# Kernel optimization log

Measured on AMD Instinct MI355X. Metric: run time of the kernel, lower is better.

Reference implementation:

```python
import jax, jax.numpy as jnp
import numpy as np

D_MODEL = 1024
NUM_HEADS = 16
D_HEAD = D_MODEL // NUM_HEADS
B, T = 2, 2048


def setup_inputs() -> dict:
    key = jax.random.key(0)
    kx, kq, kk, kv, ko = jax.random.split(key, 5)
    # xavier_uniform bound for square (D,D) linear weights
    bound = float(np.sqrt(6.0 / (D_MODEL + D_MODEL)))
    uni = lambda k: jax.random.uniform(k, (D_MODEL, D_MODEL), jnp.float32, -bound, bound)
    return {
        "x": jax.random.normal(kx, (B, T, D_MODEL), jnp.float32),
        "Wq": uni(kq),
        "Wk": uni(kk),
        "Wv": uni(kv),
        "Wo": uni(ko),
    }


def _split_heads(x):
    # (B, T, D) -> (B, H, T, d_head)
    b, t, _ = x.shape
    return x.reshape(b, t, NUM_HEADS, D_HEAD).transpose(0, 2, 1, 3)


def _exclusive_output_mod(Y, V):
    dt = V.dtype
    tiny = jnp.asarray(jnp.finfo(dt).tiny, dt)
    eps = jnp.asarray(jnp.finfo(dt).eps, dt)
    v_sq = jnp.sum(V * V, axis=-1, keepdims=True)
    y_dot_v = jnp.sum(Y * V, axis=-1, keepdims=True)
    scale = jnp.where(v_sq > 0, y_dot_v / jnp.maximum(v_sq, tiny), jnp.zeros_like(y_dot_v))
    Z = Y - scale * V
    residual_norm = jnp.linalg.norm(Z, axis=-1, keepdims=True)
    reference_norm = jnp.maximum(
        jnp.linalg.norm(Y, axis=-1, keepdims=True),
        jnp.linalg.norm(V, axis=-1, keepdims=True),
    )
    cleanup_tol = eps * Z.shape[-1] * reference_norm
    return jnp.where((v_sq > 0) & (residual_norm <= cleanup_tol), jnp.zeros_like(Z), Z)


def reference(x, Wq, Wk, Wv, Wo):
    Q = _split_heads(x @ Wq.T)  # (B,H,T,dh)
    K = _split_heads(x @ Wk.T)
    V = _split_heads(x @ Wv.T)
    sm_scale = 1.0 / np.sqrt(D_HEAD)
    scores = jnp.einsum("bhqd,bhkd->bhqk", Q, K) * sm_scale
    P = jax.nn.softmax(scores, axis=-1)
    Y = jnp.einsum("bhqk,bhkd->bhqd", P, V)
    Z = _exclusive_output_mod(Y, V)
    # merge heads: (B,H,T,dh) -> (B,T,D)
    Zm = Z.transpose(0, 2, 1, 3).reshape(x.shape[0], x.shape[1], D_MODEL)
    return Zm @ Wo.T
```

## Files before the change

### kernel.cpp

```cpp
#include <hip/hip_runtime.h>
#include <math.h>

#define DM   1024
#define TTOK 2048
#define NTOK 4096

typedef __bf16 bf16x8 __attribute__((ext_vector_type(8)));
typedef __bf16 bf16x4 __attribute__((ext_vector_type(4)));
typedef __bf16 bf16x2 __attribute__((ext_vector_type(2)));
typedef float  f32x4  __attribute__((ext_vector_type(4)));
typedef float  f32x16 __attribute__((ext_vector_type(16)));

#define QSCALE 0.18033688011112042f

#if defined(__has_builtin)
#if __has_builtin(__builtin_amdgcn_exp2f)
#define EXP2F(x) __builtin_amdgcn_exp2f(x)
#endif
#endif
#ifndef EXP2F
#define EXP2F(x) exp2f(x)
#endif

#define GLDS16(g, l) __builtin_amdgcn_global_load_lds( \
    (__attribute__((address_space(1))) void*)(g),      \
    (__attribute__((address_space(3))) void*)(l), 16, 0, 0)

__device__ __forceinline__ unsigned pk2(float a, float b) {
    bf16x2 t; t[0] = (__bf16)a; t[1] = (__bf16)b;
    return __builtin_bit_cast(unsigned, t);
}
union FU { unsigned u[4]; bf16x8 v; };

__global__ __launch_bounds__(256)
void cvt_all(const float* __restrict__ x,  const float* __restrict__ Wq,
             const float* __restrict__ Wk, const float* __restrict__ Wv,
             const float* __restrict__ Wo, __bf16* __restrict__ dst) {
    size_t g = ((size_t)blockIdx.x * 256 + threadIdx.x) * 8;
    const float* s;
    size_t off;
    const size_t NX = (size_t)NTOK * DM;
    if (g < NX) { s = x; off = g; }
    else {
        size_t gg = g - NX;
        int w = (int)(gg >> 20);
        off = gg & ((1u << 20) - 1);
        s = (w == 0) ? Wq : (w == 1) ? Wk : (w == 2) ? Wv : Wo;
    }
    float4 a = *(const float4*)(s + off);
    float4 b = *(const float4*)(s + off + 4);
    bf16x8 v;
    v[0] = (__bf16)a.x; v[1] = (__bf16)a.y; v[2] = (__bf16)a.z; v[3] = (__bf16)a.w;
    v[4] = (__bf16)b.x; v[5] = (__bf16)b.y; v[6] = (__bf16)b.z; v[7] = (__bf16)b.w;
    *(bf16x8*)(dst + g) = v;
}

#define LSTR 136
#define DBUF 8192

__global__ __launch_bounds__(256)
void gemm_qkv(const __bf16* __restrict__ X,
              const __bf16* __restrict__ W0, const __bf16* __restrict__ W1,
              const __bf16* __restrict__ W2,
              __bf16* __restrict__ Oq, __bf16* __restrict__ Ok,
              __bf16* __restrict__ Ovt)
{
    const int z = blockIdx.z;
    const __bf16 *A, *B;
    int m0, n0;
    if (z < 2) {
        A = z ? W1 : W0; B = X;
        m0 = blockIdx.y * 128; n0 = blockIdx.x * 128;
    } else {
        A = X; B = W2;
        m0 = blockIdx.x * 128; n0 = blockIdx.y * 128;
    }

    __shared__ __attribute__((aligned(16))) __bf16 smem[128 * LSTR];

    const int tid  = threadIdx.x;
    const int lane = tid & 63;
    const int wave = tid >> 6;
    const int wm = wave & 1, wn = wave >> 1;
    const int col = lane & 15, quad = lane >> 4;

    const __bf16* Ag = A + (size_t)(m0 + (tid >> 2)) * DM + (tid & 3) * 8;
    const __bf16* Bg = B + (size_t)(n0 + (tid >> 2)) * DM + (tid & 3) * 8;
    __bf16* lA = smem + tid * 8;
    __bf16* lB = smem + 4096 + tid * 8;

    f32x4 acc[4][4];
#pragma unroll
    for (int i = 0; i < 4; ++i)
#pragma unroll
        for (int j = 0; j < 4; ++j)
#pragma unroll
            for (int r = 0; r < 4; ++r) acc[i][j][r] = 0.0f;

    GLDS16(Ag,                   lA);
    GLDS16(Ag + (size_t)64 * DM, lA + 2048);
    GLDS16(Bg,                   lB);
    GLDS16(Bg + (size_t)64 * DM, lB + 2048);
    __syncthreads();

    const int nk = DM / 32;
    for (int t = 0; t < nk; ++t) {
        const int cur = (t & 1) * DBUF;
        const int nxt = DBUF - cur;

        if (t + 1 < nk) {
            const int k1 = (t + 1) * 32;
            GLDS16(Ag + k1,                   lA + nxt);
            GLDS16(Ag + (size_t)64 * DM + k1, lA + nxt + 2048);
            GLDS16(Bg + k1,                   lB + nxt);
            GLDS16(Bg + (size_t)64 * DM + k1, lB + nxt + 2048);
        }

        const __bf16* Asr = smem + cur;
        const __bf16* Bsr = smem + cur + 4096;
        bf16x8 af[4], bfr[4];
#pragma unroll
        for (int i = 0; i < 4; ++i)
            af[i] = *(const bf16x8*)&Asr[(wm * 64 + i * 16 + col) * 32 + quad * 8];
#pragma unroll
        for (int j = 0; j < 4; ++j)
            bfr[j] = *(const bf16x8*)&Bsr[(wn * 64 + j * 16 + col) * 32 + quad * 8];
#pragma unroll
        for (int i = 0; i < 4; ++i)
#pragma unroll
            for (int j = 0; j < 4; ++j)
                acc[i][j] = __builtin_amdgcn_mfma_f32_16x16x32_bf16(af[i], bfr[j], acc[i][j], 0, 0, 0);

        __syncthreads();
    }

    const float sc = (z == 0) ? QSCALE : 1.0f;
#pragma unroll
    for (int i = 0; i < 4; ++i)
#pragma unroll
        for (int j = 0; j < 4; ++j) {
            const int ml = wm * 64 + i * 16 + quad * 4;
            const int nl = wn * 64 + j * 16 + col;
            bf16x4 pk;
#pragma unroll
            for (int r = 0; r < 4; ++r) pk[r] = (__bf16)(acc[i][j][r] * sc);
            *(bf16x4*)&smem[nl * LSTR + ml] = pk;
        }
    __syncthreads();

#pragma unroll
    for (int it = 0; it < 8; ++it) {
        int c   = tid + 256 * it;
        int row = c >> 4;
        int ch  = (c & 15) * 8;
        bf16x8 v = *(const bf16x8*)&smem[row * LSTR + ch];
        if (z < 2) {
            int t  = n0 + row;
            int b  = t >> 11; t &= 2047;
            int hd = m0 + ch;
            int h  = hd >> 6, d = hd & 63;
            *(bf16x8*)&((z ? Ok : Oq)[(((size_t)(b * 16 + h)) * TTOK + t) * 64 + d]) = v;
        } else {
            int hd = n0 + row;
            int h  = hd >> 6, d = hd & 63;
            int t  = m0 + ch;
            int b  = t >> 11; t &= 2047;
            *(bf16x8*)&Ovt[(((size_t)(b * 16 + h)) * 64 + d) * TTOK + t] = v;
        }
    }
}

#define ODBUF 6144

__global__ __launch_bounds__(256)
void gemm_oproj(const __bf16* __restrict__ X, const __bf16* __restrict__ Wo,
                float* __restrict__ Of)
{
    const int f = blockIdx.x + 8 * blockIdx.y;
    const int c = f & 7, i0 = f >> 3;
    const int m0 = (8 * c + (i0 & 7)) * 64;
    const int n0 = (i0 >> 3) * 128;

    __shared__ __attribute__((aligned(16))) __bf16 smem[2 * ODBUF];

    const int tid  = threadIdx.x;
    const int lane = tid & 63;
    const int wave = tid >> 6;
    const int col = lane & 15, quad = lane >> 4;

    const __bf16* Ag = X  + (size_t)(m0 + (tid >> 2)) * DM + (tid & 3) * 8;
    const __bf16* Bg = Wo + (size_t)(n0 + (tid >> 2)) * DM + (tid & 3) * 8;
    __bf16* lA = smem + tid * 8;
    __bf16* lB = smem + 2048 + tid * 8;

    f32x4 acc[4][2];
#pragma unroll
    for (int i = 0; i < 4; ++i)
#pragma unroll
        for (int j = 0; j < 2; ++j)
#pragma unroll
            for (int r = 0; r < 4; ++r) acc[i][j][r] = 0.0f;

    GLDS16(Ag,                   lA);
    GLDS16(Bg,                   lB);
    GLDS16(Bg + (size_t)64 * DM, lB + 2048);
    __syncthreads();

    const int nk = DM / 32;
    for (int t = 0; t < nk; ++t) {
        const int cur = (t & 1) * ODBUF;
        const int nxt = ODBUF - cur;
        if (t + 1 < nk) {
            const int k1 = (t + 1) * 32;
            GLDS16(Ag + k1,                   lA + nxt);
            GLDS16(Bg + k1,                   lB + nxt);
            GLDS16(Bg + (size_t)64 * DM + k1, lB + nxt + 2048);
        }
        const __bf16* Asr = smem + cur;
        const __bf16* Bsr = smem + cur + 2048;
        bf16x8 af[4], bfr[2];
#pragma unroll
        for (int i = 0; i < 4; ++i)
            af[i] = *(const bf16x8*)&Asr[(i * 16 + col) * 32 + quad * 8];
#pragma unroll
        for (int j = 0; j < 2; ++j)
            bfr[j] = *(const bf16x8*)&Bsr[(wave * 32 + j * 16 + col) * 32 + quad * 8];
#pragma unroll
        for (int i = 0; i < 4; ++i)
#pragma unroll
            for (int j = 0; j < 2; ++j)
                acc[i][j] = __builtin_amdgcn_mfma_f32_16x16x32_bf16(af[i], bfr[j], acc[i][j], 0, 0, 0);
        __syncthreads();
    }

#pragma unroll
    for (int i = 0; i < 4; ++i)
#pragma unroll
        for (int j = 0; j < 2; ++j) {
            const int mb = m0 + i * 16 + quad * 4;
            const int n  = n0 + wave * 32 + j * 16 + col;
#pragma unroll
            for (int r = 0; r < 4; ++r)
                Of[(size_t)(mb + r) * DM + n] = acc[i][j][r];
        }
}

__global__ __launch_bounds__(256)
void attn_mfma(const __bf16* __restrict__ Qg, const __bf16* __restrict__ Kg,
               const __bf16* __restrict__ Vtg, __bf16* __restrict__ Zm)
{
    const int bh = blockIdx.y;
    const int q0 = blockIdx.x * 128;
    const size_t base = (size_t)bh * TTOK * 64;

    __shared__ __attribute__((aligned(16))) __bf16 Ks[2][64 * 72];
    __shared__ __attribute__((aligned(16))) __bf16 Vs[2][64 * 72];

    const int tid  = threadIdx.x;
    const int lane = tid & 63, wave = tid >> 6;
    const int c32  = lane & 31, h32 = lane >> 5;

    bf16x8 qf[4];
    const __bf16* qrow = Qg + base + (size_t)(q0 + wave * 32 + c32) * 64 + h32 * 8;
#pragma unroll
    for (int st = 0; st < 4; ++st)
        qf[st] = *(const bf16x8*)(qrow + st * 16);

    f32x16 O[2];
#pragma unroll
    for (int r = 0; r < 16; ++r) { O[0][r] = 0.0f; O[1][r] = 0.0f; }
    float lsum = 0.0f;

    const int rs = tid >> 2, soff = (tid & 3) * 16;

    bf16x8 kr0 = *(const bf16x8*)(Kg  + base + (size_t)rs * 64 + soff);
    bf16x8 kr1 = *(const bf16x8*)(Kg  + base + (size_t)rs * 64 + soff + 8);
    bf16x8 vr0 = *(const bf16x8*)(Vtg + base + (size_t)rs * TTOK + soff);
    bf16x8 vr1 = *(const bf16x8*)(Vtg + base + (size_t)rs * TTOK + soff + 8);
    *(bf16x8*)&Ks[0][rs * 72 + soff]     = kr0;
    *(bf16x8*)&Ks[0][rs * 72 + soff + 8] = kr1;
    *(bf16x8*)&Vs[0][rs * 72 + soff]     = vr0;
    *(bf16x8*)&Vs[0][rs * 72 + soff + 8] = vr1;
    {
        const __bf16* kp = Kg  + base + (size_t)(64 + rs) * 64 + soff;
        const __bf16* vp = Vtg + base + (size_t)rs * TTOK + 64 + soff;
        kr0 = *(const bf16x8*)(kp); kr1 = *(const bf16x8*)(kp + 8);
        vr0 = *(const bf16x8*)(vp); vr1 = *(const bf16x8*)(vp + 8);
    }
    __syncthreads();

    const int kb_tgt = (q0 >> 6) + (wave >> 1);
    const int qo     = (wave & 1) * 32 + c32;
    float vq[2][16];

    for (int kb = 0; kb < TTOK / 64; ++kb) {
        const int cur = kb & 1;
        const __bf16* Kc = Ks[cur];
        const __bf16* Vc = Vs[cur];

        f32x16 s0, s1;
#pragma unroll
        for (int r = 0; r < 16; ++r) { s0[r] = 0.0f; s1[r] = 0.0f; }
#pragma unroll
        for (int st = 0; st < 4; ++st) {
            bf16x8 a0 = *(const bf16x8*)&Kc[(c32)      * 72 + h32 * 8 + st * 16];
            bf16x8 a1 = *(const bf16x8*)&Kc[(32 + c32) * 72 + h32 * 8 + st * 16];
            s0 = __builtin_amdgcn_mfma_f32_32x32x16_bf16(a0, qf[st], s0, 0, 0, 0);
            s1 = __builtin_amdgcn_mfma_f32_32x32x16_bf16(a1, qf[st], s1, 0, 0, 0);
        }

        float pl0[16], pl1[16];
#pragma unroll
        for (int r = 0; r < 16; ++r) { pl0[r] = EXP2F(s0[r]); pl1[r] = EXP2F(s1[r]); }
#pragma unroll
        for (int r = 0; r < 16; ++r) lsum += pl0[r] + pl1[r];

        bf16x8 pf[4];
#pragma unroll
        for (int ks = 0; ks < 4; ++ks) {
            const float* pl = (ks & 2) ? pl1 : pl0;
            const int rb = (ks & 1) * 8;
            unsigned A0 = pk2(pl[rb + 0], pl[rb + 1]);
            unsigned A1 = pk2(pl[rb + 2], pl[rb + 3]);
            unsigned B0 = pk2(pl[rb + 4], pl[rb + 5]);
            unsigned B1 = pk2(pl[rb + 6], pl[rb + 7]);
            unsigned s0w = h32 ? A0 : B0;
            unsigned s1w = h32 ? A1 : B1;
            unsigned r0 = __shfl_xor(s0w, 32, 64);
            unsigned r1 = __shfl_xor(s1w, 32, 64);
            FU fu;
            fu.u[0] = h32 ? r0 : A0;
            fu.u[1] = h32 ? r1 : A1;
            fu.u[2] = h32 ? B0 : r0;
            fu.u[3] = h32 ? B1 : r1;
            pf[ks] = fu.v;
        }

#pragma unroll
        for (int ks = 0; ks < 4; ++ks) {
            bf16x8 v0 = *(const bf16x8*)&Vc[(c32)      * 72 + h32 * 8 + ks * 16];
            bf16x8 v1 = *(const bf16x8*)&Vc[(32 + c32) * 72 + h32 * 8 + ks * 16];
            O[0] = __builtin_amdgcn_mfma_f32_32x32x16_bf16(v0, pf[ks], O[0], 0, 0, 0);
            O[1] = __builtin_amdgcn_mfma_f32_32x32x16_bf16(v1, pf[ks], O[1], 0, 0, 0);
        }

        if (kb == kb_tgt) {
#pragma unroll
            for (int db = 0; db < 2; ++db)
#pragma unroll
                for (int rg = 0; rg < 16; ++rg) {
                    int d = db * 32 + (rg & 3) + 8 * (rg >> 2) + 4 * h32;
                    vq[db][rg] = (float)Vc[d * 72 + qo];
                }
        }

        __bf16* Kn = Ks[cur ^ 1];
        __bf16* Vn = Vs[cur ^ 1];
        *(bf16x8*)&Kn[rs * 72 + soff]     = kr0;
        *(bf16x8*)&Kn[rs * 72 + soff + 8] = kr1;
        *(bf16x8*)&Vn[rs * 72 + soff]     = vr0;
        *(bf16x8*)&Vn[rs * 72 + soff + 8] = vr1;

        {
            int kbn = (kb + 2) & (TTOK / 64 - 1);
            const __bf16* kp = Kg  + base + (size_t)(kbn * 64 + rs) * 64 + soff;
            const __bf16* vp = Vtg + base + (size_t)rs * TTOK + kbn * 64 + soff;
            kr0 = *(const bf16x8*)(kp); kr1 = *(const bf16x8*)(kp + 8);
            vr0 = *(const bf16x8*)(vp); vr1 = *(const bf16x8*)(vp + 8);
        }

        __syncthreads();
    }

    const float ltot = lsum + __shfl_xor(lsum, 32, 64);
    const float inv  = 1.0f / ltot;

    const int b = bh >> 4, h = bh & 15;
    const int q = q0 + wave * 32 + c32;
    float y[2][16];
    float yv = 0.f, v2 = 0.f, yy = 0.f;
#pragma unroll
    for (int db = 0; db < 2; ++db)
#pragma unroll
        for (int rg = 0; rg < 16; ++rg) {
            float yval = O[db][rg] * inv;
            float vval = vq[db][rg];
            y[db][rg] = yval;
            yv += yval * vval; v2 += vval * vval; yy += yval * yval;
        }
    yv += __shfl_xor(yv, 32, 64);
    v2 += __shfl_xor(v2, 32, 64);
    yy += __shfl_xor(yy, 32, 64);
    float scl = (v2 > 0.0f) ? yv / fmaxf(v2, 1.1754943508222875e-38f) : 0.0f;
    float zz = 0.f;
    float zvv[2][16];
#pragma unroll
    for (int db = 0; db < 2; ++db)
#pragma unroll
        for (int rg = 0; rg < 16; ++rg) {
            zvv[db][rg] = y[db][rg] - scl * vq[db][rg];
            zz += zvv[db][rg] * zvv[db][rg];
        }
    zz += __shfl_xor(zz, 32, 64);
    float znorm = sqrtf(zz);
    float refn  = fmaxf(sqrtf(yy), sqrtf(v2));
    bool  wipe  = (v2 > 0.0f) && (znorm <= 1.1920928955078125e-07f * 64.0f * refn);
#pragma unroll
    for (int db = 0; db < 2; ++db)
#pragma unroll
        for (int g = 0; g < 4; ++g) {
            bf16x4 pk;
#pragma unroll
            for (int r = 0; r < 4; ++r)
                pk[r] = (__bf16)(wipe ? 0.0f : zvv[db][4 * g + r]);
            int d = db * 32 + 8 * g + 4 * h32;
            *(bf16x4*)&Zm[((size_t)(b * TTOK + q)) * DM + h * 64 + d] = pk;
        }
}

extern "C" void kernel_launch(void* const* d_in, const int* in_sizes, int n_in,
                              void* d_out, int out_size, void* d_ws, size_t ws_size,
                              hipStream_t stream) {
    const float* x  = (const float*)d_in[0];
    const float* Wq = (const float*)d_in[1];
    const float* Wk = (const float*)d_in[2];
    const float* Wv = (const float*)d_in[3];
    const float* Wo = (const float*)d_in[4];

    const size_t NX = (size_t)NTOK * DM;
    const size_t NW = (size_t)DM * DM;
    __bf16* xb  = (__bf16*)d_ws;
    __bf16* wqb = xb  + NX;
    __bf16* wkb = wqb + NW;
    __bf16* wvb = wkb + NW;
    __bf16* wob = wvb + NW;
    __bf16* Qb  = wob + NW;
    __bf16* Kb  = Qb  + NX;
    __bf16* Vtb = Kb  + NX;
    __bf16* Zmb = Vtb + NX;

    cvt_all<<<(NX + 4 * NW) / 2048, 256, 0, stream>>>(x, Wq, Wk, Wv, Wo, xb);

    gemm_qkv<<<dim3(32, 8, 3), 256, 0, stream>>>(
        xb, wqb, wkb, wvb, Qb, Kb, Vtb);

    attn_mfma<<<dim3(TTOK / 128, 32), 256, 0, stream>>>(Qb, Kb, Vtb, Zmb);

    gemm_oproj<<<dim3(8, 64), 256, 0, stream>>>(Zmb, wob, (float*)d_out);
}
```

Baseline: 185.7 us.

## Split attention KV range across two wave groups and merge partial outputs via LDS

Each attention block now runs 512 threads: two groups of four waves each cover half of the key/value sequence for the same 128 queries, each with its own double-buffered LDS tiles. After the loop the second group writes its partial O accumulators and row sums to LDS and the first group adds them before normalising. The V self-row values used by the exclusive-output step are now read directly from global memory instead of being captured during the loop. The softmax exp/pack is also interleaved with the PV MFMAs. This aims to double the waves in flight per block to hide latency, at the cost of more LDS per block, an extra reduction pass, and tighter register pressure under launch_bounds(512,4).

New measurement: 184.6 us. No clear change (-0.6%).

```diff
diff --git a/kernel.cpp b/kernel.cpp
--- a/kernel.cpp
+++ b/kernel.cpp
@@ -245,7 +245,7 @@
         }
 }
 
-__global__ __launch_bounds__(256)
+__global__ __launch_bounds__(512, 4)
 void attn_mfma(const __bf16* __restrict__ Qg, const __bf16* __restrict__ Kg,
                const __bf16* __restrict__ Vtg, __bf16* __restrict__ Zm)
 {
@@ -253,15 +253,17 @@
     const int q0 = blockIdx.x * 128;
     const size_t base = (size_t)bh * TTOK * 64;
 
-    __shared__ __attribute__((aligned(16))) __bf16 Ks[2][64 * 72];
-    __shared__ __attribute__((aligned(16))) __bf16 Vs[2][64 * 72];
+    __shared__ __attribute__((aligned(16))) __bf16 lds[2][2][2][64 * 72];
 
     const int tid  = threadIdx.x;
-    const int lane = tid & 63, wave = tid >> 6;
+    const int lane = tid & 63;
+    const int wave = tid >> 6;
+    const int half = wave >> 2;
+    const int qw   = wave & 3;
     const int c32  = lane & 31, h32 = lane >> 5;
 
     bf16x8 qf[4];
-    const __bf16* qrow = Qg + base + (size_t)(q0 + wave * 32 + c32) * 64 + h32 * 8;
+    const __bf16* qrow = Qg + base + (size_t)(q0 + qw * 32 + c32) * 64 + h32 * 8;
 #pragma unroll
     for (int st = 0; st < 4; ++st)
         qf[st] = *(const bf16x8*)(qrow + st * 16);
@@ -271,32 +273,36 @@
     for (int r = 0; r < 16; ++r) { O[0][r] = 0.0f; O[1][r] = 0.0f; }
     float lsum = 0.0f;
 
-    const int rs = tid >> 2, soff = (tid & 3) * 16;
-
-    bf16x8 kr0 = *(const bf16x8*)(Kg  + base + (size_t)rs * 64 + soff);
-    bf16x8 kr1 = *(const bf16x8*)(Kg  + base + (size_t)rs * 64 + soff + 8);
-    bf16x8 vr0 = *(const bf16x8*)(Vtg + base + (size_t)rs * TTOK + soff);
-    bf16x8 vr1 = *(const bf16x8*)(Vtg + base + (size_t)rs * TTOK + soff + 8);
-    *(bf16x8*)&Ks[0][rs * 72 + soff]     = kr0;
-    *(bf16x8*)&Ks[0][rs * 72 + soff + 8] = kr1;
-    *(bf16x8*)&Vs[0][rs * 72 + soff]     = vr0;
-    *(bf16x8*)&Vs[0][rs * 72 + soff + 8] = vr1;
+    const int tid8 = tid & 255;
+    const int rs   = tid8 >> 2;
+    const int soff = (tid8 & 3) * 16;
+    const int kb0  = half * 1024;
+
     {
-        const __bf16* kp = Kg  + base + (size_t)(64 + rs) * 64 + soff;
-        const __bf16* vp = Vtg + base + (size_t)rs * TTOK + 64 + soff;
+        const __bf16* kp = Kg  + base + (size_t)(kb0 + rs) * 64 + soff;
+        const __bf16* vp = Vtg + base + (size_t)rs * TTOK + kb0 + soff;
+        bf16x8 k0 = *(const bf16x8*)(kp);
+        bf16x8 k1 = *(const bf16x8*)(kp + 8);
+        bf16x8 v0 = *(const bf16x8*)(vp);
+        bf16x8 v1 = *(const bf16x8*)(vp + 8);
+        *(bf16x8*)&lds[half][0][0][rs * 72 + soff]     = k0;
+        *(bf16x8*)&lds[half][0][0][rs * 72 + soff + 8] = k1;
+        *(bf16x8*)&lds[half][1][0][rs * 72 + soff]     = v0;
+        *(bf16x8*)&lds[half][1][0][rs * 72 + soff + 8] = v1;
+    }
+    bf16x8 kr0, kr1, vr0, vr1;
+    {
+        const __bf16* kp = Kg  + base + (size_t)(kb0 + 64 + rs) * 64 + soff;
+        const __bf16* vp = Vtg + base + (size_t)rs * TTOK + kb0 + 64 + soff;
         kr0 = *(const bf16x8*)(kp); kr1 = *(const bf16x8*)(kp + 8);
         vr0 = *(const bf16x8*)(vp); vr1 = *(const bf16x8*)(vp + 8);
     }
     __syncthreads();
 
-    const int kb_tgt = (q0 >> 6) + (wave >> 1);
-    const int qo     = (wave & 1) * 32 + c32;
-    float vq[2][16];
-
-    for (int kb = 0; kb < TTOK / 64; ++kb) {
-        const int cur = kb & 1;
-        const __bf16* Kc = Ks[cur];
-        const __bf16* Vc = Vs[cur];
+    for (int it = 0; it < 16; ++it) {
+        const int cur = it & 1;
+        const __bf16* Kc = &lds[half][0][cur][0];
+        const __bf16* Vc = &lds[half][1][cur][0];
 
         f32x16 s0, s1;
 #pragma unroll
@@ -309,21 +315,17 @@
             s1 = __builtin_amdgcn_mfma_f32_32x32x16_bf16(a1, qf[st], s1, 0, 0, 0);
         }
 
-        float pl0[16], pl1[16];
-#pragma unroll
-        for (int r = 0; r < 16; ++r) { pl0[r] = EXP2F(s0[r]); pl1[r] = EXP2F(s1[r]); }
-#pragma unroll
-        for (int r = 0; r < 16; ++r) lsum += pl0[r] + pl1[r];
-
-        bf16x8 pf[4];
 #pragma unroll
         for (int ks = 0; ks < 4; ++ks) {
-            const float* pl = (ks & 2) ? pl1 : pl0;
+            const f32x16& sv = (ks & 2) ? s1 : s0;
             const int rb = (ks & 1) * 8;
-            unsigned A0 = pk2(pl[rb + 0], pl[rb + 1]);
-            unsigned A1 = pk2(pl[rb + 2], pl[rb + 3]);
-            unsigned B0 = pk2(pl[rb + 4], pl[rb + 5]);
-            unsigned B1 = pk2(pl[rb + 6], pl[rb + 7]);
+            float p0 = EXP2F(sv[rb + 0]), p1 = EXP2F(sv[rb + 1]);
+            float p2 = EXP2F(sv[rb + 2]), p3 = EXP2F(sv[rb + 3]);
+            float p4 = EXP2F(sv[rb + 4]), p5 = EXP2F(sv[rb + 5]);
+            float p6 = EXP2F(sv[rb + 6]), p7 = EXP2F(sv[rb + 7]);
+            lsum += ((p0 + p1) + (p2 + p3)) + ((p4 + p5) + (p6 + p7));
+            unsigned A0 = pk2(p0, p1), A1 = pk2(p2, p3);
+            unsigned B0 = pk2(p4, p5), B1 = pk2(p6, p7);
             unsigned s0w = h32 ? A0 : B0;
             unsigned s1w = h32 ? A1 : B1;
             unsigned r0 = __shfl_xor(s0w, 32, 64);
@@ -333,38 +335,21 @@
             fu.u[1] = h32 ? r1 : A1;
             fu.u[2] = h32 ? B0 : r0;
             fu.u[3] = h32 ? B1 : r1;
-            pf[ks] = fu.v;
-        }
-
-#pragma unroll
-        for (int ks = 0; ks < 4; ++ks) {
             bf16x8 v0 = *(const bf16x8*)&Vc[(c32)      * 72 + h32 * 8 + ks * 16];
             bf16x8 v1 = *(const bf16x8*)&Vc[(32 + c32) * 72 + h32 * 8 + ks * 16];
-            O[0] = __builtin_amdgcn_mfma_f32_32x32x16_bf16(v0, pf[ks], O[0], 0, 0, 0);
-            O[1] = __builtin_amdgcn_mfma_f32_32x32x16_bf16(v1, pf[ks], O[1], 0, 0, 0);
-        }
-
-        if (kb == kb_tgt) {
-#pragma unroll
-            for (int db = 0; db < 2; ++db)
-#pragma unroll
-                for (int rg = 0; rg < 16; ++rg) {
-                    int d = db * 32 + (rg & 3) + 8 * (rg >> 2) + 4 * h32;
-                    vq[db][rg] = (float)Vc[d * 72 + qo];
-                }
-        }
-
-        __bf16* Kn = Ks[cur ^ 1];
-        __bf16* Vn = Vs[cur ^ 1];
-        *(bf16x8*)&Kn[rs * 72 + soff]     = kr0;
-        *(bf16x8*)&Kn[rs * 72 + soff + 8] = kr1;
-        *(bf16x8*)&Vn[rs * 72 + soff]     = vr0;
-        *(bf16x8*)&Vn[rs * 72 + soff + 8] = vr1;
+            O[0] = __builtin_amdgcn_mfma_f32_32x32x16_bf16(v0, fu.v, O[0], 0, 0, 0);
+            O[1] = __builtin_amdgcn_mfma_f32_32x32x16_bf16(v1, fu.v, O[1], 0, 0, 0);
+        }
+
+        *(bf16x8*)&lds[half][0][cur ^ 1][rs * 72 + soff]     = kr0;
+        *(bf16x8*)&lds[half][0][cur ^ 1][rs * 72 + soff + 8] = kr1;
+        *(bf16x8*)&lds[half][1][cur ^ 1][rs * 72 + soff]     = vr0;
+        *(bf16x8*)&lds[half][1][cur ^ 1][rs * 72 + soff + 8] = vr1;
 
         {
-            int kbn = (kb + 2) & (TTOK / 64 - 1);
-            const __bf16* kp = Kg  + base + (size_t)(kbn * 64 + rs) * 64 + soff;
-            const __bf16* vp = Vtg + base + (size_t)rs * TTOK + kbn * 64 + soff;
+            int itn = (it + 2) & 15;
+            const __bf16* kp = Kg  + base + (size_t)(kb0 + itn * 64 + rs) * 64 + soff;
+            const __bf16* vp = Vtg + base + (size_t)rs * TTOK + kb0 + itn * 64 + soff;
             kr0 = *(const bf16x8*)(kp); kr1 = *(const bf16x8*)(kp + 8);
             vr0 = *(const bf16x8*)(vp); vr1 = *(const bf16x8*)(vp + 8);
         }
@@ -372,11 +357,35 @@
         __syncthreads();
     }
 
+    float* cb = (float*)&lds[0][0][0][0];
+    if (wave >= 4) {
+        float* me = cb + qw * 2048 + lane * 32;
+#pragma unroll
+        for (int r = 0; r < 16; ++r) { me[r] = O[0][r]; me[16 + r] = O[1][r]; }
+        cb[8192 + qw * 64 + lane] = lsum;
+    }
+    __syncthreads();
+    if (wave >= 4) return;
+    {
+        const float* pr = cb + qw * 2048 + lane * 32;
+#pragma unroll
+        for (int r = 0; r < 16; ++r) { O[0][r] += pr[r]; O[1][r] += pr[16 + r]; }
+        lsum += cb[8192 + qw * 64 + lane];
+    }
     const float ltot = lsum + __shfl_xor(lsum, 32, 64);
     const float inv  = 1.0f / ltot;
 
+    const int q = q0 + qw * 32 + c32;
+    float vq[2][16];
+#pragma unroll
+    for (int db = 0; db < 2; ++db)
+#pragma unroll
+        for (int rg = 0; rg < 16; ++rg) {
+            int d = db * 32 + (rg & 3) + 8 * (rg >> 2) + 4 * h32;
+            vq[db][rg] = (float)Vtg[base + (size_t)d * TTOK + q];
+        }
+
     const int b = bh >> 4, h = bh & 15;
-    const int q = q0 + wave * 32 + c32;
     float y[2][16];
     float yv = 0.f, v2 = 0.f, yy = 0.f;
 #pragma unroll
@@ -444,7 +453,7 @@
     gemm_qkv<<<dim3(32, 8, 3), 256, 0, stream>>>(
         xb, wqb, wkb, wvb, Qb, Kb, Vtb);
 
-    attn_mfma<<<dim3(TTOK / 128, 32), 256, 0, stream>>>(Qb, Kb, Vtb, Zmb);
+    attn_mfma<<<dim3(TTOK / 128, 32), 512, 0, stream>>>(Qb, Kb, Vtb, Zmb);
 
     gemm_oproj<<<dim3(8, 64), 256, 0, stream>>>(Zmb, wob, (float*)d_out);
 }
```
